# Optimization experiments

Measured on AMD Instinct MI355X. Metric: run time of the kernel, lower is better.

## Reference

```python
import jax, jax.numpy as jnp
import numpy as np

B, S, E, H = 2, 2048, 1024, 16
DH = E // H


def setup_inputs() -> dict:
    key = jax.random.key(0)
    ks = jax.random.split(key, 12)
    std = 1.0 / np.sqrt(E)
    inp = {
        "query": jax.random.normal(ks[0], (B, S, E), jnp.float32),
        "key": jax.random.normal(ks[1], (B, S, E), jnp.float32),
        "value": jax.random.normal(ks[2], (B, S, E), jnp.float32),
        "mask": jax.random.randint(ks[3], (B, 1, 1, S), 0, 2, jnp.int32),
        "Wq": jax.random.normal(ks[4], (E, E), jnp.float32) * std,
        "bq": jnp.zeros((E,), jnp.float32),
        "Wk": jax.random.normal(ks[5], (E, E), jnp.float32) * std,
        "bk": jnp.zeros((E,), jnp.float32),
        "Wv": jax.random.normal(ks[6], (E, E), jnp.float32) * std,
        "bv": jnp.zeros((E,), jnp.float32),
        "Wo": jax.random.normal(ks[7], (E, E), jnp.float32) * std,
        "bo": jnp.zeros((E,), jnp.float32),
    }
    return inp


def reference(query, key, value, mask, Wq, bq, Wk, bk, Wv, bv, Wo, bo):
    b = query.shape[0]
    # QKV projections, then split heads: [B,S,E] -> [B,H,S,Dh]
    def split_heads(x):
        return x.reshape(b, -1, H, DH).transpose(0, 2, 1, 3)
    q = split_heads(query @ Wq + bq)
    k = split_heads(key @ Wk + bk)
    v = split_heads(value @ Wv + bv)
    # explicit bmm -> mask -> softmax -> bmm (non-SDPA), scores [B,H,Sq,Sk]
    scores = jnp.einsum("bhqd,bhkd->bhqk", q, k) / np.sqrt(DH).astype(np.float32)
    scores = jnp.where(mask == 0, jnp.float32(-1e9), scores)
    attn = jax.nn.softmax(scores, axis=-1)  # dropout is identity in eval mode
    out = jnp.einsum("bhqk,bhkd->bhqd", attn, v)
    out = out.transpose(0, 2, 1, 3).reshape(b, -1, E)  # merge heads
    return out @ Wo + bo
```

## Files before the change

kernel.cpp:

```cpp
#include <hip/hip_runtime.h>
#include <hip/hip_bf16.h>
#include <stdint.h>

#define B_ 2
#define S_ 2048
#define E_ 1024
#define H_ 16
#define DH_ 64
#define MELEMS (4096 * 1024)
#define WE (1024 * 1024)

typedef unsigned short u16;
typedef __bf16 bf16x8 __attribute__((ext_vector_type(8)));
typedef u16 u16x8 __attribute__((ext_vector_type(8)));
typedef u16 u16x4 __attribute__((ext_vector_type(4)));
typedef float f32x4 __attribute__((ext_vector_type(4)));
typedef float f32x16 __attribute__((ext_vector_type(16)));
typedef uint32_t u32x4 __attribute__((ext_vector_type(4)));
typedef uint32_t u32x2v __attribute__((ext_vector_type(2)));

__device__ __forceinline__ float bf2f(u16 u) {
    union { uint32_t i; float f; } v; v.i = ((uint32_t)u) << 16; return v.f;
}
__device__ __forceinline__ u16 f2bf(float f) {
    union { float f; uint32_t i; } v; v.f = f;
    uint32_t r = (v.i + 0x7FFFu + ((v.i >> 16) & 1u)) >> 16;
    return (u16)r;
}
__device__ __forceinline__ uint32_t pkbf(float a, float b) {
    __hip_bfloat162 h = __float22bfloat162_rn(make_float2(a, b));
    uint32_t r; __builtin_memcpy(&r, &h, 4);
    return r;
}
__device__ __forceinline__ bf16x8 ldfrag(const u16* p) {
    u16x8 t = *(const u16x8*)p;
    return __builtin_bit_cast(bf16x8, t);
}
__device__ __forceinline__ void gld16(const void* g, void* l) {
    __builtin_amdgcn_global_load_lds(
        (const __attribute__((address_space(1))) void*)g,
        (__attribute__((address_space(3))) void*)l, 16, 0, 0);
}

__global__ __launch_bounds__(256)
void cvt_all(const float* __restrict__ q, const float* __restrict__ k,
             const float* __restrict__ v,
             const float* __restrict__ W0, const float* __restrict__ W1,
             const float* __restrict__ W2, const float* __restrict__ W3,
             u16* __restrict__ Qi, u16* __restrict__ Ki, u16* __restrict__ Vi,
             u16* __restrict__ T0, u16* __restrict__ T1,
             u16* __restrict__ T2, u16* __restrict__ T3)
{
    __shared__ float tile[64][65];
    const int bid = blockIdx.x;
    const int tid = threadIdx.x;

    if (bid < 6144) {
        const int z = bid >> 11;
        const int cx = bid & 2047;
        const float* src = (z == 0) ? q : (z == 1) ? k : v;
        u16* dst = (z == 0) ? Qi : (z == 1) ? Ki : Vi;
        const size_t i8 = ((size_t)cx * 256 + tid) * 8;
        float4 f0 = *(const float4*)&src[i8];
        float4 f1 = *(const float4*)&src[i8 + 4];
        u16x8 t;
        t[0] = f2bf(f0.x); t[1] = f2bf(f0.y); t[2] = f2bf(f0.z); t[3] = f2bf(f0.w);
        t[4] = f2bf(f1.x); t[5] = f2bf(f1.y); t[6] = f2bf(f1.z); t[7] = f2bf(f1.w);
        *(u16x8*)&dst[i8] = t;
    } else {
        const int rr = bid - 6144;
        const int z = rr >> 8;
        const int tt = rr & 255;
        const float* W = (z == 0) ? W0 : (z == 1) ? W1 : (z == 2) ? W2 : W3;
        u16* T = (z == 0) ? T0 : (z == 1) ? T1 : (z == 2) ? T2 : T3;
        const int n0 = (tt & 15) * 64, k0 = (tt >> 4) * 64;
        const int r = tid >> 2, c0 = (tid & 3) * 16;

        #pragma unroll
        for (int i = 0; i < 4; ++i) {
            float4 w = *(const float4*)&W[(size_t)(k0 + r) * 1024 + n0 + c0 + i * 4];
            tile[r][c0 + i * 4 + 0] = w.x; tile[r][c0 + i * 4 + 1] = w.y;
            tile[r][c0 + i * 4 + 2] = w.z; tile[r][c0 + i * 4 + 3] = w.w;
        }
        __syncthreads();
        u16x8 a, b;
        #pragma unroll
        for (int j = 0; j < 8; ++j) a[j] = f2bf(tile[c0 + j][r]);
        #pragma unroll
        for (int j = 0; j < 8; ++j) b[j] = f2bf(tile[c0 + 8 + j][r]);
        *(u16x8*)&T[(size_t)(n0 + r) * 1024 + k0 + c0] = a;
        *(u16x8*)&T[(size_t)(n0 + r) * 1024 + k0 + c0 + 8] = b;
    }
}

template<int BN>
__global__ __launch_bounds__(256)
void gemm_bt(const u16* __restrict__ A0, const u16* __restrict__ A1,
             const u16* __restrict__ A2,
             const u16* __restrict__ Bt0, const u16* __restrict__ Bt1,
             const u16* __restrict__ Bt2,
             const float* __restrict__ b0, const float* __restrict__ b1,
             const float* __restrict__ b2,
             void* __restrict__ C0, void* __restrict__ C1, void* __restrict__ C2,
             const int* __restrict__ mask,
             int c_f32, int vt_z, float scale0, int K)
{
    const int z = blockIdx.z;
    const u16* A  = (z == 0) ? A0 : (z == 1) ? A1 : A2;
    const u16* Bt = (z == 0) ? Bt0 : (z == 1) ? Bt1 : Bt2;
    const float* bias = (z == 0) ? b0 : (z == 1) ? b1 : b2;
    void* C = (z == 0) ? C0 : (z == 1) ? C1 : C2;
    const float scale = (z == 0) ? scale0 : 1.0f;

    __shared__ alignas(16) u16 As[128 * 32];
    __shared__ alignas(16) u16 Bs[BN * 32];

    const int tid  = threadIdx.x;
    const int lane = tid & 63;
    const int wv   = tid >> 6;
    const int l15  = lane & 15;
    const int quad = lane >> 4;
    const int m0 = blockIdx.y * 128;
    const int n0 = blockIdx.x * BN;
    const int wr = (wv >> 1) * 64;
    const int wc = (wv & 1) * (BN / 2);

    const int srow = wv * 16 + (lane >> 2);
    const int skk  = (lane & 3) * 8;

    constexpr int NJ = BN / 32;
    f32x4 acc[4][NJ] = {};

    for (int k0 = 0; k0 < K; k0 += 32) {
        __syncthreads();
        #pragma unroll
        for (int h = 0; h < 2; ++h) {
            const int r = h * 64 + srow;
            gld16(&A[(size_t)(m0 + r) * K + k0 + skk], &As[r * 32 + skk]);
        }
        #pragma unroll
        for (int h = 0; h < BN / 64; ++h) {
            const int r = h * 64 + srow;
            gld16(&Bt[(size_t)(n0 + r) * K + k0 + skk], &Bs[r * 32 + skk]);
        }
        __syncthreads();

        bf16x8 a[4], b[NJ];
        #pragma unroll
        for (int i = 0; i < 4; ++i)
            a[i] = ldfrag(&As[(wr + i * 16 + l15) * 32 + quad * 8]);
        #pragma unroll
        for (int j = 0; j < NJ; ++j)
            b[j] = ldfrag(&Bs[(wc + j * 16 + l15) * 32 + quad * 8]);
        #pragma unroll
        for (int i = 0; i < 4; ++i)
            #pragma unroll
            for (int j = 0; j < NJ; ++j)
                acc[i][j] = __builtin_amdgcn_mfma_f32_16x16x32_bf16(
                    a[i], b[j], acc[i][j], 0, 0, 0);
    }

    #pragma unroll
    for (int j = 0; j < NJ; ++j) {
        const int col = n0 + wc + j * 16 + l15;
        const float bcol = bias[col];
        #pragma unroll
        for (int i = 0; i < 4; ++i) {
            if (z == vt_z) {
                const int row0 = m0 + wr + i * 16 + quad * 4;
                const int bb = row0 >> 11, s0 = row0 & 2047;
                const int4 mv = *(const int4*)&mask[bb * S_ + s0];
                u16x4 t;
                t[0] = mv.x ? f2bf((acc[i][j][0] + bcol) * scale) : (u16)0;
                t[1] = mv.y ? f2bf((acc[i][j][1] + bcol) * scale) : (u16)0;
                t[2] = mv.z ? f2bf((acc[i][j][2] + bcol) * scale) : (u16)0;
                t[3] = mv.w ? f2bf((acc[i][j][3] + bcol) * scale) : (u16)0;
                *(u16x4*)&((u16*)C)[((size_t)bb * E_ + col) * S_ + s0] = t;
            } else {
                #pragma unroll
                for (int r = 0; r < 4; ++r) {
                    const int row = m0 + wr + i * 16 + quad * 4 + r;
                    const float v = (acc[i][j][r] + bcol) * scale;
                    if (c_f32) ((float*)C)[(size_t)row * 1024 + col] = v;
                    else       ((u16*)C)[(size_t)row * 1024 + col]  = f2bf(v);
                }
            }
        }
    }
}

__global__ __launch_bounds__(512, 4)
void attn_v8(const u16* __restrict__ Q, const u16* __restrict__ K,
             const u16* __restrict__ Vt_g, const int* __restrict__ mask,
             u16* __restrict__ ctx)
{
    __shared__ alignas(16) u16 smem[2][16384];
    __shared__ alignas(16) u16 Mbf[S_];

    const int tid  = threadIdx.x;
    const int lane = tid & 63;
    const int wv   = tid >> 6;
    const int l31  = lane & 31;
    const int half = lane >> 5;
    const int sw7  = lane & 7;
    const int qw   = wv & 3;
    const int kh   = wv >> 2;
    const int kbase = kh * 64;
    const int qt = blockIdx.x;
    const int bh = blockIdx.y;
    const int b  = bh >> 4, h = bh & 15;

    const size_t qk_off = (size_t)b * S_ * E_ + (size_t)h * DH_;
    const size_t vt_off = ((size_t)b * E_ + (size_t)h * DH_) * S_;
    const int* mrow = &mask[b * S_];

    {
        const int i = tid * 4;
        const int4 m = *(const int4*)&mrow[i];
        u16x4 t;
        t[0] = m.x ? (u16)0x3F80 : (u16)0;
        t[1] = m.y ? (u16)0x3F80 : (u16)0;
        t[2] = m.z ? (u16)0x3F80 : (u16)0;
        t[3] = m.w ? (u16)0x3F80 : (u16)0;
        *(u16x4*)&Mbf[i] = t;
    }

    const int q0 = qt * 128 + qw * 32;
    bf16x8 qf[4];
    #pragma unroll
    for (int s = 0; s < 4; ++s)
        qf[s] = ldfrag(&Q[qk_off + (size_t)(q0 + l31) * E_ + s * 16 + half * 8]);

    f32x16 O[2] = {};
    f32x16 La  = {};

    auto stage = [&](int kc, int buf) {
        u16* Kb = &smem[buf][0];
        u16* Vb = &smem[buf][8192];
        #pragma unroll
        for (int g = 0; g < 2; ++g) {
            const int key = g * 64 + (tid >> 3);
            const int ks  = tid & 7;
            const int kd  = ks ^ (key & 7);
            gld16(&K[qk_off + (size_t)(kc + key) * E_ + kd * 8],
                  &Kb[key * 64 + ks * 8]);
        }
        #pragma unroll
        for (int g = 0; g < 2; ++g) {
            const int d  = g * 32 + (tid >> 4);
            const int vs = tid & 15;
            const int kb = (vs & 8) | ((vs & 7) ^ (d & 7));
            gld16(&Vt_g[vt_off + (size_t)d * S_ + kc + kb * 8],
                  &Vb[d * 128 + vs * 8]);
        }
    };

    stage(0, 0);
    int cur = 0;

    for (int kc = 0; kc < S_; kc += 128) {
        __syncthreads();
        if (kc + 128 < S_) stage(kc + 128, cur ^ 1);
        const u16* Kb = &smem[cur][0];
        const u16* Vb = &smem[cur][8192];

        #pragma unroll
        for (int kt = 0; kt < 2; ++kt) {
            f32x16 St = {};
            #pragma unroll
            for (int s = 0; s < 4; ++s) {
                bf16x8 kf = ldfrag(&Kb[(kbase + kt * 32 + l31) * 64 +
                                       ((s * 2 + half) ^ sw7) * 8]);
                St = __builtin_amdgcn_mfma_f32_32x32x16_bf16(kf, qf[s], St, 0, 0, 0);
            }
            float ex[16];
            #pragma unroll
            for (int i = 0; i < 16; ++i) ex[i] = __builtin_exp2f(St[i]);
            const uint32_t w0 = pkbf(ex[0], ex[1]),  w1 = pkbf(ex[2], ex[3]);
            const uint32_t w2 = pkbf(ex[4], ex[5]),  w3 = pkbf(ex[6], ex[7]);
            const uint32_t w4 = pkbf(ex[8], ex[9]),  w5 = pkbf(ex[10], ex[11]);
            const uint32_t w6 = pkbf(ex[12], ex[13]), w7 = pkbf(ex[14], ex[15]);
            u32x2v r02 = __builtin_amdgcn_permlane32_swap(w0, w2, false, false);
            u32x2v r13 = __builtin_amdgcn_permlane32_swap(w1, w3, false, false);
            u32x2v r46 = __builtin_amdgcn_permlane32_swap(w4, w6, false, false);
            u32x2v r57 = __builtin_amdgcn_permlane32_swap(w5, w7, false, false);
            u32x4 f0, f1;
            f0[0] = r02[0]; f0[1] = r13[0]; f0[2] = r02[1]; f0[3] = r13[1];
            f1[0] = r46[0]; f1[1] = r57[0]; f1[2] = r46[1]; f1[3] = r57[1];
            const bf16x8 pa0 = __builtin_bit_cast(bf16x8, f0);
            const bf16x8 pa1 = __builtin_bit_cast(bf16x8, f1);

            {
                bf16x8 mb0 = ldfrag(&Mbf[kc + kbase + kt * 32 + half * 8]);
                bf16x8 mb1 = ldfrag(&Mbf[kc + kbase + kt * 32 + 16 + half * 8]);
                La = __builtin_amdgcn_mfma_f32_32x32x16_bf16(pa0, mb0, La, 0, 0, 0);
                La = __builtin_amdgcn_mfma_f32_32x32x16_bf16(pa1, mb1, La, 0, 0, 0);
            }
            #pragma unroll
            for (int nt = 0; nt < 2; ++nt) {
                const int drow = nt * 32 + l31;
                const int kb0 = kh * 8 + kt * 4 + half;
                const int kb1 = kh * 8 + kt * 4 + 2 + half;
                bf16x8 vb0 = ldfrag(&Vb[drow * 128 +
                                        ((kb0 & 8) | ((kb0 & 7) ^ sw7)) * 8]);
                bf16x8 vb1 = ldfrag(&Vb[drow * 128 +
                                        ((kb1 & 8) | ((kb1 & 7) ^ sw7)) * 8]);
                O[nt] = __builtin_amdgcn_mfma_f32_32x32x16_bf16(pa0, vb0, O[nt], 0, 0, 0);
                O[nt] = __builtin_amdgcn_mfma_f32_32x32x16_bf16(pa1, vb1, O[nt], 0, 0, 0);
            }
        }
        cur ^= 1;
    }

    __syncthreads();
    float* scr = (float*)smem;
    const int sbase = (qw * 64 + lane) * 49;
    if (kh == 1) {
        #pragma unroll
        for (int i = 0; i < 16; ++i) scr[sbase + i]      = O[0][i];
        #pragma unroll
        for (int i = 0; i < 16; ++i) scr[sbase + 16 + i] = O[1][i];
        #pragma unroll
        for (int i = 0; i < 16; ++i) scr[sbase + 32 + i] = La[i];
    }
    __syncthreads();
    if (kh == 0) {
        #pragma unroll
        for (int nt = 0; nt < 2; ++nt)
            #pragma unroll
            for (int i = 0; i < 16; ++i) {
                const float o = O[nt][i] + scr[sbase + nt * 16 + i];
                const float l = La[i]    + scr[sbase + 32 + i];
                const int q = q0 + (i & 3) + 8 * (i >> 2) + 4 * half;
                const int e = h * DH_ + nt * 32 + l31;
                ctx[((size_t)b * S_ + q) * E_ + e] = f2bf(o / l);
            }
    }
}

__global__ __launch_bounds__(256)
void gemm_bias(const void* __restrict__ A, int a_f32,
               const float* __restrict__ W, const float* __restrict__ bias,
               void* __restrict__ C, int c_f32,
               int M, int N, int K, float scale)
{
    __shared__ alignas(16) u16 As[64 * 32];
    __shared__ alignas(16) u16 Wt[64 * 32];
    const int tid  = threadIdx.x;
    const int lane = tid & 63;
    const int wv   = tid >> 6;
    const int l15  = lane & 15;
    const int quad = lane >> 4;
    const int m0 = blockIdx.y * 64, n0 = blockIdx.x * 64;
    const int wr = (wv >> 1) * 32, wc = (wv & 1) * 32;
    const int ar = tid >> 2, ac = (tid & 3) * 8;
    const int wk = tid >> 3, wn = (tid & 7) * 8;
    f32x4 acc[2][2] = {};
    for (int k0 = 0; k0 < K; k0 += 32) {
        __syncthreads();
        if (a_f32) {
            const float* Af = (const float*)A;
            const float* p = &Af[(size_t)(m0 + ar) * K + k0 + ac];
            float4 f0 = *(const float4*)p; float4 f1 = *(const float4*)(p + 4);
            u16x8 t;
            t[0] = f2bf(f0.x); t[1] = f2bf(f0.y); t[2] = f2bf(f0.z); t[3] = f2bf(f0.w);
            t[4] = f2bf(f1.x); t[5] = f2bf(f1.y); t[6] = f2bf(f1.z); t[7] = f2bf(f1.w);
            *(u16x8*)&As[ar * 32 + ac] = t;
        } else {
            const u16* Ab = (const u16*)A;
            *(u16x8*)&As[ar * 32 + ac] = *(const u16x8*)&Ab[(size_t)(m0 + ar) * K + k0 + ac];
        }
        {
            const float* p = &W[(size_t)(k0 + wk) * N + n0 + wn];
            float4 g0 = *(const float4*)p; float4 g1 = *(const float4*)(p + 4);
            float fv[8] = {g0.x, g0.y, g0.z, g0.w, g1.x, g1.y, g1.z, g1.w};
            #pragma unroll
            for (int j = 0; j < 8; ++j) Wt[(wn + j) * 32 + wk] = f2bf(fv[j]);
        }
        __syncthreads();
        bf16x8 a[2], b[2];
        #pragma unroll
        for (int sm = 0; sm < 2; ++sm) a[sm] = ldfrag(&As[(wr + sm * 16 + l15) * 32 + quad * 8]);
        #pragma unroll
        for (int sn = 0; sn < 2; ++sn) b[sn] = ldfrag(&Wt[(wc + sn * 16 + l15) * 32 + quad * 8]);
        #pragma unroll
        for (int sm = 0; sm < 2; ++sm)
            #pragma unroll
            for (int sn = 0; sn < 2; ++sn)
                acc[sm][sn] = __builtin_amdgcn_mfma_f32_16x16x32_bf16(a[sm], b[sn], acc[sm][sn], 0, 0, 0);
    }
    #pragma unroll
    for (int sm = 0; sm < 2; ++sm)
        #pragma unroll
        for (int sn = 0; sn < 2; ++sn) {
            const int col = n0 + wc + sn * 16 + l15;
            const float bcol = bias[col];
            #pragma unroll
            for (int r = 0; r < 4; ++r) {
                const int row = m0 + wr + sm * 16 + quad * 4 + r;
                const float v = (acc[sm][sn][r] + bcol) * scale;
                if (c_f32) ((float*)C)[(size_t)row * N + col] = v;
                else       ((u16*)C)[(size_t)row * N + col]  = f2bf(v);
            }
        }
}

__global__ __launch_bounds__(256)
void attn_v2(const u16* __restrict__ Q, const u16* __restrict__ K,
             const u16* __restrict__ V, const int* __restrict__ mask,
             u16* __restrict__ ctx, int BH_per_B)
{
    __shared__ alignas(16) u16 Ks[64 * 72];
    __shared__ alignas(16) u16 Vt[64 * 72];
    __shared__ alignas(16) u16 Pb[4][16 * 72];
    const int tid  = threadIdx.x;
    const int lane = tid & 63;
    const int wv   = tid >> 6;
    const int l15  = lane & 15;
    const int quad = lane >> 4;
    const int qt = blockIdx.x;
    const int bh = blockIdx.y;
    const int b  = bh / BH_per_B, h = bh % BH_per_B;
    const size_t headoff = (size_t)b * S_ * E_ + (size_t)h * DH_;
    const int qrow = qt * 64 + wv * 16 + l15;
    const bf16x8 qf0 = ldfrag(&Q[headoff + (size_t)qrow * E_ + quad * 8]);
    const bf16x8 qf1 = ldfrag(&Q[headoff + (size_t)qrow * E_ + 32 + quad * 8]);
    f32x4 oacc[4] = {};
    float mrun[4] = {-1e30f, -1e30f, -1e30f, -1e30f};
    float lrun[4] = {0.f, 0.f, 0.f, 0.f};
    const int skey = tid >> 2;
    const int sd0  = (tid & 3) * 16;
    for (int kc = 0; kc < S_; kc += 64) {
        __syncthreads();
        {
            const u16* kg = &K[headoff + (size_t)(kc + skey) * E_ + sd0];
            *(u16x8*)&Ks[skey * 72 + sd0]     = *(const u16x8*)kg;
            *(u16x8*)&Ks[skey * 72 + sd0 + 8] = *(const u16x8*)(kg + 8);
            const u16* vg = &V[headoff + (size_t)(kc + skey) * E_ + sd0];
            u16x8 v0 = *(const u16x8*)vg;
            u16x8 v1 = *(const u16x8*)(vg + 8);
            #pragma unroll
            for (int j = 0; j < 8; ++j) {
                const int d = sd0 + j;
                Vt[d * 72 + (skey ^ (((d >> 3) & 7) * 8))] = v0[j];
            }
            #pragma unroll
            for (int j = 0; j < 8; ++j) {
                const int d = sd0 + 8 + j;
                Vt[d * 72 + (skey ^ (((d >> 3) & 7) * 8))] = v1[j];
            }
        }
        __syncthreads();
        f32x4 sb[4];
        #pragma unroll
        for (int t = 0; t < 4; ++t) {
            bf16x8 kf0 = ldfrag(&Ks[(t * 16 + l15) * 72 + quad * 8]);
            bf16x8 kf1 = ldfrag(&Ks[(t * 16 + l15) * 72 + 32 + quad * 8]);
            f32x4 s = {};
            s = __builtin_amdgcn_mfma_f32_16x16x32_bf16(qf0, kf0, s, 0, 0, 0);
            s = __builtin_amdgcn_mfma_f32_16x16x32_bf16(qf1, kf1, s, 0, 0, 0);
            const int mv = mask[b * S_ + kc + t * 16 + l15];
            #pragma unroll
            for (int r = 0; r < 4; ++r) sb[t][r] = (mv == 0) ? -1e9f : s[r];
        }
        #pragma unroll
        for (int r = 0; r < 4; ++r) {
            float m = fmaxf(fmaxf(sb[0][r], sb[1][r]), fmaxf(sb[2][r], sb[3][r]));
            #pragma unroll
            for (int off = 1; off < 16; off <<= 1) m = fmaxf(m, __shfl_xor(m, off));
            const float mnew  = fmaxf(mrun[r], m);
            const float alpha = __expf(mrun[r] - mnew);
            mrun[r] = mnew;
            float sum = 0.f;
            #pragma unroll
            for (int t = 0; t < 4; ++t) {
                const float p = __expf(sb[t][r] - mnew);
                sb[t][r] = p; sum += p;
            }
            #pragma unroll
            for (int off = 1; off < 16; off <<= 1) sum += __shfl_xor(sum, off);
            lrun[r] = lrun[r] * alpha + sum;
            #pragma unroll
            for (int c = 0; c < 4; ++c) oacc[c][r] *= alpha;
        }
        #pragma unroll
        for (int t = 0; t < 4; ++t)
            #pragma unroll
            for (int r = 0; r < 4; ++r)
                Pb[wv][(quad * 4 + r) * 72 + t * 16 + l15] = f2bf(sb[t][r]);
        const bf16x8 pa0 = ldfrag(&Pb[wv][l15 * 72 + quad * 8]);
        const bf16x8 pa1 = ldfrag(&Pb[wv][l15 * 72 + 32 + quad * 8]);
        #pragma unroll
        for (int c = 0; c < 4; ++c) {
            const int d = c * 16 + l15;
            const int sg = ((d >> 3) & 7) * 8;
            bf16x8 vb0 = ldfrag(&Vt[d * 72 + ((quad * 8) ^ sg)]);
            bf16x8 vb1 = ldfrag(&Vt[d * 72 + ((32 + quad * 8) ^ sg)]);
            oacc[c] = __builtin_amdgcn_mfma_f32_16x16x32_bf16(pa0, vb0, oacc[c], 0, 0, 0);
            oacc[c] = __builtin_amdgcn_mfma_f32_16x16x32_bf16(pa1, vb1, oacc[c], 0, 0, 0);
        }
    }
    #pragma unroll
    for (int c = 0; c < 4; ++c) {
        const int e = h * DH_ + c * 16 + l15;
        #pragma unroll
        for (int r = 0; r < 4; ++r) {
            const int qg = qt * 64 + wv * 16 + quad * 4 + r;
            ctx[((size_t)b * S_ + qg) * E_ + e] = f2bf(oacc[c][r] / lrun[r]);
        }
    }
}

extern "C" void kernel_launch(void* const* d_in, const int* in_sizes, int n_in,
                              void* d_out, int out_size, void* d_ws, size_t ws_size,
                              hipStream_t stream)
{
    const float* query = (const float*)d_in[0];
    const float* key   = (const float*)d_in[1];
    const float* value = (const float*)d_in[2];
    const int*   mask  = (const int*)d_in[3];
    const float* Wq = (const float*)d_in[4];  const float* bq = (const float*)d_in[5];
    const float* Wk = (const float*)d_in[6];  const float* bk = (const float*)d_in[7];
    const float* Wv = (const float*)d_in[8];  const float* bv = (const float*)d_in[9];
    const float* Wo = (const float*)d_in[10]; const float* bo = (const float*)d_in[11];
    float* out = (float*)d_out;

    u16* ws = (u16*)d_ws;
    dim3 blk(256);

    const size_t need_fancy = (size_t)(6 * MELEMS + 4 * WE) * sizeof(u16);
    const size_t need_full  = (size_t)(4 * MELEMS) * sizeof(u16) + 64;

    if (ws_size >= need_fancy) {
        u16* Qi  = ws;
        u16* Ki  = Qi + MELEMS;
        u16* Vi  = Ki + MELEMS;
        u16* Wqt = Vi + MELEMS;
        u16* Wkt = Wqt + WE;
        u16* Wvt = Wkt + WE;
        u16* Wot = Wvt + WE;
        u16* Qp  = Wot + WE;
        u16* Kp  = Qp + MELEMS;
        u16* Vp  = Kp + MELEMS;
        u16* Cp  = Qi;

        cvt_all<<<dim3(7168), blk, 0, stream>>>(query, key, value,
                                                Wq, Wk, Wv, Wo,
                                                Qi, Ki, Vi, Wqt, Wkt, Wvt, Wot);

        gemm_bt<128><<<dim3(8, 32, 3), blk, 0, stream>>>(
            Qi, Ki, Vi, Wqt, Wkt, Wvt, bq, bk, bv,
            Qp, Kp, Vp, mask, 0, 2, 0.125f * 1.44269504f, E_);

        attn_v8<<<dim3(S_ / 128, B_ * H_), dim3(512), 0, stream>>>(
            Qp, Kp, Vp, mask, Cp);

        gemm_bt<64><<<dim3(16, 32, 1), blk, 0, stream>>>(
            Cp, Cp, Cp, Wot, Wot, Wot, bo, bo, bo,
            out, out, out, mask, 1, -1, 1.0f, E_);
    } else if (ws_size >= need_full) {
        u16* Qp = ws;
        u16* Kp = ws + MELEMS;
        u16* Vp = ws + 2 * MELEMS;
        u16* Cp = ws + 3 * MELEMS;
        const int M = B_ * S_;
        dim3 gg(E_ / 64, M / 64);
        gemm_bias<<<gg, blk, 0, stream>>>(query, 1, Wq, bq, Qp, 0, M, E_, E_, 0.125f);
        gemm_bias<<<gg, blk, 0, stream>>>(key,   1, Wk, bk, Kp, 0, M, E_, E_, 1.0f);
        gemm_bias<<<gg, blk, 0, stream>>>(value, 1, Wv, bv, Vp, 0, M, E_, E_, 1.0f);
        attn_v2<<<dim3(S_ / 64, B_ * H_), blk, 0, stream>>>(Qp, Kp, Vp, mask, Cp, H_);
        gemm_bias<<<gg, blk, 0, stream>>>(Cp, 0, Wo, bo, out, 1, M, E_, E_, 1.0f);
    } else {
        const size_t szb = (size_t)S_ * E_;
        u16* Qp = ws; u16* Kp = ws + szb; u16* Vp = ws + 2 * szb; u16* Cp = ws + 3 * szb;
        dim3 gg(E_ / 64, S_ / 64);
        for (int b = 0; b < B_; ++b) {
            gemm_bias<<<gg, blk, 0, stream>>>(query + b * szb, 1, Wq, bq, Qp, 0, S_, E_, E_, 0.125f);
            gemm_bias<<<gg, blk, 0, stream>>>(key   + b * szb, 1, Wk, bk, Kp, 0, S_, E_, E_, 1.0f);
            gemm_bias<<<gg, blk, 0, stream>>>(value + b * szb, 1, Wv, bv, Vp, 0, S_, E_, E_, 1.0f);
            attn_v2<<<dim3(S_ / 64, H_), blk, 0, stream>>>(Qp, Kp, Vp, mask + b * S_, Cp, H_);
            gemm_bias<<<gg, blk, 0, stream>>>(Cp, 0, Wo, bo, ((float*)d_out) + b * szb, 1, S_, E_, E_, 1.0f);
        }
    }
}
```

Measured before the change: 154.0 us.

## Halve attention key chunk to 64, raise occupancy, vectorize cross-wave reduction

The attention kernel now stages 64 keys per iteration instead of 128, halving the shared-memory double buffer, and raises the launch-bounds occupancy hint from 4 to 6 blocks per CU. The final reduction between the two key-half wave groups now writes swizzled float4 rows and shares the row-sum only once per row through a small extra buffer. The bf16 pack uses inline v_cvt_pk_bf16_f32 assembly instead of the HIP intrinsic. The aim is more resident blocks and cheaper conversion and epilogue work, at the cost of twice as many loop iterations and barriers per key sweep and a tighter register budget.

```diff
diff --git a/kernel.cpp b/kernel.cpp
--- a/kernel.cpp
+++ b/kernel.cpp
@@ -27,9 +27,9 @@
     uint32_t r = (v.i + 0x7FFFu + ((v.i >> 16) & 1u)) >> 16;
     return (u16)r;
 }
-__device__ __forceinline__ uint32_t pkbf(float a, float b) {
-    __hip_bfloat162 h = __float22bfloat162_rn(make_float2(a, b));
-    uint32_t r; __builtin_memcpy(&r, &h, 4);
+__device__ __forceinline__ uint32_t cvtpk(float a, float b) {
+    uint32_t r;
+    asm("v_cvt_pk_bf16_f32 %0, %1, %2" : "=v"(r) : "v"(a), "v"(b));
     return r;
 }
 __device__ __forceinline__ bf16x8 ldfrag(const u16* p) {
@@ -166,8 +166,8 @@
         const float bcol = bias[col];
         #pragma unroll
         for (int i = 0; i < 4; ++i) {
+            const int row0 = m0 + wr + i * 16 + quad * 4;
             if (z == vt_z) {
-                const int row0 = m0 + wr + i * 16 + quad * 4;
                 const int bb = row0 >> 11, s0 = row0 & 2047;
                 const int4 mv = *(const int4*)&mask[bb * S_ + s0];
                 u16x4 t;
@@ -179,7 +179,7 @@
             } else {
                 #pragma unroll
                 for (int r = 0; r < 4; ++r) {
-                    const int row = m0 + wr + i * 16 + quad * 4 + r;
+                    const int row = row0 + r;
                     const float v = (acc[i][j][r] + bcol) * scale;
                     if (c_f32) ((float*)C)[(size_t)row * 1024 + col] = v;
                     else       ((u16*)C)[(size_t)row * 1024 + col]  = f2bf(v);
@@ -189,13 +189,14 @@
     }
 }
 
-__global__ __launch_bounds__(512, 4)
-void attn_v8(const u16* __restrict__ Q, const u16* __restrict__ K,
-             const u16* __restrict__ Vt_g, const int* __restrict__ mask,
-             u16* __restrict__ ctx)
+__global__ __launch_bounds__(512, 6)
+void attn_v11(const u16* __restrict__ Q, const u16* __restrict__ K,
+              const u16* __restrict__ Vt_g, const int* __restrict__ mask,
+              u16* __restrict__ ctx)
 {
-    __shared__ alignas(16) u16 smem[2][16384];
+    __shared__ alignas(16) u16 smem[2][8192];
     __shared__ alignas(16) u16 Mbf[S_];
+    __shared__ float scrl[256];
 
     const int tid  = threadIdx.x;
     const int lane = tid & 63;
@@ -205,7 +206,7 @@
     const int sw7  = lane & 7;
     const int qw   = wv & 3;
     const int kh   = wv >> 2;
-    const int kbase = kh * 64;
+    const int kbase = kh * 32;
     const int qt = blockIdx.x;
     const int bh = blockIdx.y;
     const int b  = bh >> 4, h = bh & 15;
@@ -232,109 +233,108 @@
         qf[s] = ldfrag(&Q[qk_off + (size_t)(q0 + l31) * E_ + s * 16 + half * 8]);
 
     f32x16 O[2] = {};
-    f32x16 La  = {};
+    f32x16 lacc = {};
 
     auto stage = [&](int kc, int buf) {
-        u16* Kb = &smem[buf][0];
-        u16* Vb = &smem[buf][8192];
-        #pragma unroll
-        for (int g = 0; g < 2; ++g) {
-            const int key = g * 64 + (tid >> 3);
-            const int ks  = tid & 7;
-            const int kd  = ks ^ (key & 7);
-            gld16(&K[qk_off + (size_t)(kc + key) * E_ + kd * 8],
-                  &Kb[key * 64 + ks * 8]);
-        }
-        #pragma unroll
-        for (int g = 0; g < 2; ++g) {
-            const int d  = g * 32 + (tid >> 4);
-            const int vs = tid & 15;
-            const int kb = (vs & 8) | ((vs & 7) ^ (d & 7));
-            gld16(&Vt_g[vt_off + (size_t)d * S_ + kc + kb * 8],
-                  &Vb[d * 128 + vs * 8]);
-        }
+        const int rr = tid >> 3;
+        const int ks = tid & 7;
+        const int gb = ks ^ (rr & 7);
+        gld16(&K[qk_off + (size_t)(kc + rr) * E_ + gb * 8],
+              &smem[buf][rr * 64 + ks * 8]);
+        gld16(&Vt_g[vt_off + (size_t)rr * S_ + kc + gb * 8],
+              &smem[buf][4096 + rr * 64 + ks * 8]);
     };
 
     stage(0, 0);
     int cur = 0;
 
-    for (int kc = 0; kc < S_; kc += 128) {
-        __syncthreads();
-        if (kc + 128 < S_) stage(kc + 128, cur ^ 1);
+    for (int kc = 0; kc < S_; kc += 64) {
+        __syncthreads();
+        if (kc + 64 < S_) stage(kc + 64, cur ^ 1);
         const u16* Kb = &smem[cur][0];
-        const u16* Vb = &smem[cur][8192];
-
-        #pragma unroll
-        for (int kt = 0; kt < 2; ++kt) {
-            f32x16 St = {};
-            #pragma unroll
-            for (int s = 0; s < 4; ++s) {
-                bf16x8 kf = ldfrag(&Kb[(kbase + kt * 32 + l31) * 64 +
-                                       ((s * 2 + half) ^ sw7) * 8]);
-                St = __builtin_amdgcn_mfma_f32_32x32x16_bf16(kf, qf[s], St, 0, 0, 0);
-            }
-            float ex[16];
-            #pragma unroll
-            for (int i = 0; i < 16; ++i) ex[i] = __builtin_exp2f(St[i]);
-            const uint32_t w0 = pkbf(ex[0], ex[1]),  w1 = pkbf(ex[2], ex[3]);
-            const uint32_t w2 = pkbf(ex[4], ex[5]),  w3 = pkbf(ex[6], ex[7]);
-            const uint32_t w4 = pkbf(ex[8], ex[9]),  w5 = pkbf(ex[10], ex[11]);
-            const uint32_t w6 = pkbf(ex[12], ex[13]), w7 = pkbf(ex[14], ex[15]);
-            u32x2v r02 = __builtin_amdgcn_permlane32_swap(w0, w2, false, false);
-            u32x2v r13 = __builtin_amdgcn_permlane32_swap(w1, w3, false, false);
-            u32x2v r46 = __builtin_amdgcn_permlane32_swap(w4, w6, false, false);
-            u32x2v r57 = __builtin_amdgcn_permlane32_swap(w5, w7, false, false);
-            u32x4 f0, f1;
-            f0[0] = r02[0]; f0[1] = r13[0]; f0[2] = r02[1]; f0[3] = r13[1];
-            f1[0] = r46[0]; f1[1] = r57[0]; f1[2] = r46[1]; f1[3] = r57[1];
-            const bf16x8 pa0 = __builtin_bit_cast(bf16x8, f0);
-            const bf16x8 pa1 = __builtin_bit_cast(bf16x8, f1);
-
-            {
-                bf16x8 mb0 = ldfrag(&Mbf[kc + kbase + kt * 32 + half * 8]);
-                bf16x8 mb1 = ldfrag(&Mbf[kc + kbase + kt * 32 + 16 + half * 8]);
-                La = __builtin_amdgcn_mfma_f32_32x32x16_bf16(pa0, mb0, La, 0, 0, 0);
-                La = __builtin_amdgcn_mfma_f32_32x32x16_bf16(pa1, mb1, La, 0, 0, 0);
-            }
-            #pragma unroll
-            for (int nt = 0; nt < 2; ++nt) {
-                const int drow = nt * 32 + l31;
-                const int kb0 = kh * 8 + kt * 4 + half;
-                const int kb1 = kh * 8 + kt * 4 + 2 + half;
-                bf16x8 vb0 = ldfrag(&Vb[drow * 128 +
-                                        ((kb0 & 8) | ((kb0 & 7) ^ sw7)) * 8]);
-                bf16x8 vb1 = ldfrag(&Vb[drow * 128 +
-                                        ((kb1 & 8) | ((kb1 & 7) ^ sw7)) * 8]);
-                O[nt] = __builtin_amdgcn_mfma_f32_32x32x16_bf16(pa0, vb0, O[nt], 0, 0, 0);
-                O[nt] = __builtin_amdgcn_mfma_f32_32x32x16_bf16(pa1, vb1, O[nt], 0, 0, 0);
-            }
+        const u16* Vb = &smem[cur][4096];
+
+        f32x16 St = {};
+        #pragma unroll
+        for (int s = 0; s < 4; ++s) {
+            bf16x8 kf = ldfrag(&Kb[(kbase + l31) * 64 + ((s * 2 + half) ^ sw7) * 8]);
+            St = __builtin_amdgcn_mfma_f32_32x32x16_bf16(kf, qf[s], St, 0, 0, 0);
+        }
+        float ex[16];
+        #pragma unroll
+        for (int i = 0; i < 16; ++i) ex[i] = __builtin_exp2f(St[i]);
+
+        uint32_t wd[8];
+        #pragma unroll
+        for (int i = 0; i < 8; ++i) wd[i] = cvtpk(ex[2 * i], ex[2 * i + 1]);
+
+        u32x2v r02 = __builtin_amdgcn_permlane32_swap(wd[0], wd[2], false, false);
+        u32x2v r13 = __builtin_amdgcn_permlane32_swap(wd[1], wd[3], false, false);
+        u32x2v r46 = __builtin_amdgcn_permlane32_swap(wd[4], wd[6], false, false);
+        u32x2v r57 = __builtin_amdgcn_permlane32_swap(wd[5], wd[7], false, false);
+        u32x4 f0, f1;
+        f0[0] = r02[0]; f0[1] = r13[0]; f0[2] = r02[1]; f0[3] = r13[1];
+        f1[0] = r46[0]; f1[1] = r57[0]; f1[2] = r46[1]; f1[3] = r57[1];
+        const bf16x8 pa0 = __builtin_bit_cast(bf16x8, f0);
+        const bf16x8 pa1 = __builtin_bit_cast(bf16x8, f1);
+
+        {
+            bf16x8 mb0 = ldfrag(&Mbf[kc + kbase + half * 8]);
+            bf16x8 mb1 = ldfrag(&Mbf[kc + kbase + 16 + half * 8]);
+            lacc = __builtin_amdgcn_mfma_f32_32x32x16_bf16(pa0, mb0, lacc, 0, 0, 0);
+            lacc = __builtin_amdgcn_mfma_f32_32x32x16_bf16(pa1, mb1, lacc, 0, 0, 0);
+        }
+
+        #pragma unroll
+        for (int nt = 0; nt < 2; ++nt) {
+            const int drow = nt * 32 + l31;
+            const int kb0 = kh * 4 + half;
+            const int kb1 = kh * 4 + 2 + half;
+            bf16x8 vb0 = ldfrag(&Vb[drow * 64 + (kb0 ^ sw7) * 8]);
+            bf16x8 vb1 = ldfrag(&Vb[drow * 64 + (kb1 ^ sw7) * 8]);
+            O[nt] = __builtin_amdgcn_mfma_f32_32x32x16_bf16(pa0, vb0, O[nt], 0, 0, 0);
+            O[nt] = __builtin_amdgcn_mfma_f32_32x32x16_bf16(pa1, vb1, O[nt], 0, 0, 0);
         }
         cur ^= 1;
     }
 
     __syncthreads();
     float* scr = (float*)smem;
-    const int sbase = (qw * 64 + lane) * 49;
+    const int sbase = (qw * 64 + lane) * 32;
     if (kh == 1) {
         #pragma unroll
-        for (int i = 0; i < 16; ++i) scr[sbase + i]      = O[0][i];
-        #pragma unroll
-        for (int i = 0; i < 16; ++i) scr[sbase + 16 + i] = O[1][i];
-        #pragma unroll
-        for (int i = 0; i < 16; ++i) scr[sbase + 32 + i] = La[i];
+        for (int j = 0; j < 4; ++j) {
+            f32x4 t0, t1;
+            #pragma unroll
+            for (int r = 0; r < 4; ++r) { t0[r] = O[0][j * 4 + r]; t1[r] = O[1][j * 4 + r]; }
+            *(f32x4*)&scr[sbase + (j ^ sw7) * 4]       = t0;
+            *(f32x4*)&scr[sbase + ((j + 4) ^ sw7) * 4] = t1;
+        }
+        if (l31 == 0) {
+            #pragma unroll
+            for (int i = 0; i < 16; ++i)
+                scrl[qw * 32 + half * 16 + i] = lacc[i];
+        }
     }
     __syncthreads();
     if (kh == 0) {
         #pragma unroll
-        for (int nt = 0; nt < 2; ++nt)
-            #pragma unroll
-            for (int i = 0; i < 16; ++i) {
-                const float o = O[nt][i] + scr[sbase + nt * 16 + i];
-                const float l = La[i]    + scr[sbase + 32 + i];
-                const int q = q0 + (i & 3) + 8 * (i >> 2) + 4 * half;
-                const int e = h * DH_ + nt * 32 + l31;
-                ctx[((size_t)b * S_ + q) * E_ + e] = f2bf(o / l);
+        for (int nt = 0; nt < 2; ++nt) {
+            #pragma unroll
+            for (int j = 0; j < 4; ++j) {
+                const f32x4 p = *(const f32x4*)&scr[sbase + (((nt * 4 + j) ^ sw7)) * 4];
+                #pragma unroll
+                for (int r = 0; r < 4; ++r) {
+                    const int i  = j * 4 + r;
+                    const int ql = (i & 3) + 8 * (i >> 2) + 4 * half;
+                    const float lt = lacc[i] + scrl[qw * 32 + half * 16 + i];
+                    const float o  = O[nt][i] + p[r];
+                    const int q = q0 + ql;
+                    const int e = h * DH_ + nt * 32 + l31;
+                    ctx[((size_t)b * S_ + q) * E_ + e] = f2bf(o / lt);
+                }
             }
+        }
     }
 }
 
@@ -552,7 +552,7 @@
             Qi, Ki, Vi, Wqt, Wkt, Wvt, bq, bk, bv,
             Qp, Kp, Vp, mask, 0, 2, 0.125f * 1.44269504f, E_);
 
-        attn_v8<<<dim3(S_ / 128, B_ * H_), dim3(512), 0, stream>>>(
+        attn_v11<<<dim3(S_ / 128, B_ * H_), dim3(512), 0, stream>>>(
             Qp, Kp, Vp, mask, Cp);
 
         gemm_bt<64><<<dim3(16, 32, 1), blk, 0, stream>>>(
```

Result: slower. 362.3 us (+135.3%).
